# Kernel optimization log

Measured on AMD Instinct MI355X. Metric: run time of the kernel, lower is better.

The kernel has to match this reference:

```python
import jax, jax.numpy as jnp
import numpy as np

N = 16384
E = 524288
K = 16
IN_C, HID, OUT = 3, 64, 64


def _mlp(h, Wa, ba, Wb, bb):
    # Linear -> ReLU -> Linear -> ReLU (as in nn.Sequential)
    return jax.nn.relu(jax.nn.relu(h @ Wa + ba) @ Wb + bb)


def _edgeconv(x, src, dst, Wa, ba, Wb, bb, n):
    # PyG EdgeConv message: nn([x_i, x_j - x_i]) with i=dst (target), j=src (source)
    xi = x[dst]                       # [E, C]
    xj = x[src]                       # [E, C]
    m = _mlp(jnp.concatenate([xi, xj - xi], axis=-1), Wa, ba, Wb, bb)  # [E, H]
    out = jax.ops.segment_max(m, dst, num_segments=n)
    # nodes with no incoming edges: fill 0 (PyG scatter-max fill value)
    return jnp.where(jnp.isfinite(out), out, 0.0)


def _knn_edges(x, k):
    # pairwise squared distances in feature space; includes self (torch_cluster.knn(x, x, k))
    sq = jnp.sum(x * x, axis=1)                      # [N]
    dist = sq[:, None] + sq[None, :] - 2.0 * (x @ x.T)  # [N, N]
    _, idx = jax.lax.top_k(-dist, k)                 # [N, k] nearest (incl. self)
    src = idx.reshape(-1)
    dst = jnp.repeat(jnp.arange(x.shape[0]), k)
    return src, dst


def setup_inputs() -> dict:
    key = jax.random.key(0)
    ks = jax.random.split(key, 8)
    sc = lambda fan: 1.0 / np.sqrt(fan)
    return {
        "x": jax.random.normal(ks[0], (N, IN_C), dtype=jnp.float32),
        "edge_index": jax.random.randint(ks[1], (2, E), 0, N, dtype=jnp.int64),
        "k": K,
        "W1": jax.random.normal(ks[2], (2 * IN_C, HID), dtype=jnp.float32) * sc(2 * IN_C),
        "b1": jnp.zeros((HID,), dtype=jnp.float32),
        "W2": jax.random.normal(ks[3], (HID, HID), dtype=jnp.float32) * sc(HID),
        "b2": jnp.zeros((HID,), dtype=jnp.float32),
        "W3": jax.random.normal(ks[4], (2 * HID, OUT), dtype=jnp.float32) * sc(2 * HID),
        "b3": jnp.zeros((OUT,), dtype=jnp.float32),
        "W4": jax.random.normal(ks[5], (OUT, OUT), dtype=jnp.float32) * sc(OUT),
        "b4": jnp.zeros((OUT,), dtype=jnp.float32),
    }


def reference(x, edge_index, k, W1, b1, W2, b2, W3, b3, W4, b4):
    n = x.shape[0]
    # static EdgeConv (edge_index[0]=source j, edge_index[1]=target i)
    x1 = _edgeconv(x, edge_index[0], edge_index[1], W1, b1, W2, b2, n)
    # DynamicEdgeConv: kNN in feature space of x1, then EdgeConv
    src2, dst2 = _knn_edges(x1, k)
    x2 = _edgeconv(x1, src2, dst2, W3, b3, W4, b4, n)
    return x2
```

## Files before the change

### kernel.cpp

```cpp
#include <hip/hip_runtime.h>
#include <stdint.h>

#define NN   16384
#define NE   524288
#define TK   17
#define TAU  4e-5f

#define S1   2048
#define JC1  16
#define CH1  (S1 / JC1)
#define JCB  8
#define CAP  512
#define LCAP 64
#define OFB  256
#define MGNB2 1e-3f

typedef unsigned long long u64;
typedef unsigned int u32;
typedef unsigned short u16;
typedef __attribute__((ext_vector_type(8))) short bf16x8;
typedef __attribute__((ext_vector_type(4))) float f32x4;

__device__ __forceinline__ float mulrn(float a, float b) { return __fmul_rn(a, b); }
__device__ __forceinline__ float addrn(float a, float b) { return __fadd_rn(a, b); }
__device__ __forceinline__ float subrn(float a, float b) { return __fsub_rn(a, b); }

__device__ __forceinline__ u32 fkey(float f) {
    u32 b = __float_as_uint(f);
    return ((int)b < 0) ? ~b : (b | 0x80000000u);
}
__device__ __forceinline__ float inv_fkey(u32 k) {
    return (k & 0x80000000u) ? __uint_as_float(k & 0x7fffffffu) : __uint_as_float(~k);
}

__device__ __forceinline__ u16 f2bf(float f) {
    u32 x = __float_as_uint(f);
    u32 r = x + 0x7fffu + ((x >> 16) & 1u);
    return (u16)(r >> 16);
}

template<int K>
__device__ __forceinline__ void topk_insert(u64 (&key)[K], u64 nk) {
#pragma unroll
    for (int s = K - 1; s >= 1; --s) {
        bool c1 = nk < key[s - 1];
        bool c0 = nk < key[s];
        key[s] = c1 ? key[s - 1] : (c0 ? nk : key[s]);
    }
    if (nk < key[0]) key[0] = nk;
}

#define XR_DECL float4 xq0, xq1, xq2, xq3, xq4, xq5, xq6, xq7, \
                       xq8, xq9, xq10, xq11, xq12, xq13, xq14, xq15

#define XR_LOAD(ptr) do { const float4* xp_ = (const float4*)(ptr); \
    xq0  = xp_[0];  xq1  = xp_[1];  xq2  = xp_[2];  xq3  = xp_[3]; \
    xq4  = xp_[4];  xq5  = xp_[5];  xq6  = xp_[6];  xq7  = xp_[7]; \
    xq8  = xp_[8];  xq9  = xp_[9];  xq10 = xp_[10]; xq11 = xp_[11]; \
    xq12 = xp_[12]; xq13 = xp_[13]; xq14 = xp_[14]; xq15 = xp_[15]; } while (0)

#define DOT_STEP(res, qq, w_) \
    res = fmaf(qq.x, w_.x, res); res = fmaf(qq.y, w_.y, res); \
    res = fmaf(qq.z, w_.z, res); res = fmaf(qq.w, w_.w, res);

#define DOT64(res, ptr) do { const float4* jp_ = (const float4*)(ptr); \
    float4 w_ = jp_[0]; \
    res = mulrn(xq0.x, w_.x); res = fmaf(xq0.y, w_.y, res); \
    res = fmaf(xq0.z, w_.z, res); res = fmaf(xq0.w, w_.w, res); \
    w_ = jp_[1];  DOT_STEP(res, xq1,  w_) \
    w_ = jp_[2];  DOT_STEP(res, xq2,  w_) \
    w_ = jp_[3];  DOT_STEP(res, xq3,  w_) \
    w_ = jp_[4];  DOT_STEP(res, xq4,  w_) \
    w_ = jp_[5];  DOT_STEP(res, xq5,  w_) \
    w_ = jp_[6];  DOT_STEP(res, xq6,  w_) \
    w_ = jp_[7];  DOT_STEP(res, xq7,  w_) \
    w_ = jp_[8];  DOT_STEP(res, xq8,  w_) \
    w_ = jp_[9];  DOT_STEP(res, xq9,  w_) \
    w_ = jp_[10]; DOT_STEP(res, xq10, w_) \
    w_ = jp_[11]; DOT_STEP(res, xq11, w_) \
    w_ = jp_[12]; DOT_STEP(res, xq12, w_) \
    w_ = jp_[13]; DOT_STEP(res, xq13, w_) \
    w_ = jp_[14]; DOT_STEP(res, xq14, w_) \
    w_ = jp_[15]; DOT_STEP(res, xq15, w_) } while (0)

__global__ __launch_bounds__(256) void hist_kernel(const int* __restrict__ ei,
                                                   int* __restrict__ hist) {
    int e = blockIdx.x * 256 + threadIdx.x;
    atomicAdd(&hist[ei[NE + e]], 1);
}

__global__ __launch_bounds__(256) void scan_kernel(const int* __restrict__ hist,
                                                   int* __restrict__ base) {
    __shared__ int part[256];
    __shared__ int off[256];
    int t = threadIdx.x;
    int s = 0;
    for (int b = 0; b < 64; b++) s += hist[t * 64 + b];
    part[t] = s;
    __syncthreads();
    if (t == 0) {
        int run = 0;
        for (int i = 0; i < 256; i++) { off[i] = run; run += part[i]; }
    }
    __syncthreads();
    int run = off[t];
    for (int b = 0; b < 64; b++) {
        base[t * 64 + b] = run;
        run += hist[t * 64 + b];
    }
}

__global__ __launch_bounds__(256) void scatter_kernel(const int* __restrict__ ei,
                                                      int* __restrict__ base,
                                                      int* __restrict__ esrc,
                                                      int* __restrict__ edst) {
    int e = blockIdx.x * 256 + threadIdx.x;
    int d = ei[NE + e];
    int pos = atomicAdd(&base[d], 1);
    esrc[pos] = ei[e];
    edst[pos] = d;
}

__global__ __launch_bounds__(256) void conv1_np_kernel(const float* __restrict__ x,
                                                       const float* __restrict__ W1,
                                                       const float* __restrict__ b1,
                                                       const float* __restrict__ W2,
                                                       const float* __restrict__ b2,
                                                       const int* __restrict__ esrc,
                                                       const int* __restrict__ edst,
                                                       float* __restrict__ x1n) {
    __shared__ float HT[64 * 132];
    __shared__ float W1s[384];
    __shared__ float W2s[64 * 64];
    __shared__ float b1s[64], b2s[64];
    __shared__ int dsts[128];
    int t = threadIdx.x;
    int eb = blockIdx.x * 128;

    {
        const float4* w4 = (const float4*)W2;
        float4* wd = (float4*)W2s;
#pragma unroll
        for (int q = 0; q < 4; q++) wd[t + q * 256] = w4[t + q * 256];
        if (t < 96) ((float4*)W1s)[t] = ((const float4*)W1)[t];
        if (t < 64) { b1s[t] = b1[t]; b2s[t] = b2[t]; }
    }
    __syncthreads();

    {
        int el = t >> 1;
        int cb = (t & 1) * 32;
        int e = eb + el;
        int j = esrc[e];
        int i = edst[e];
        if ((t & 1) == 0) dsts[el] = i;
        float xi0 = x[i * 3 + 0], xi1 = x[i * 3 + 1], xi2 = x[i * 3 + 2];
        float xj0 = x[j * 3 + 0], xj1 = x[j * 3 + 1], xj2 = x[j * 3 + 2];
        float d0 = subrn(xj0, xi0), d1 = subrn(xj1, xi1), d2 = subrn(xj2, xi2);
#pragma unroll
        for (int cc = 0; cc < 32; cc++) {
            int c = cb + cc;
            float acc = mulrn(xi0, W1s[c]);
            acc = fmaf(xi1, W1s[64 + c], acc);
            acc = fmaf(xi2, W1s[128 + c], acc);
            acc = fmaf(d0,  W1s[192 + c], acc);
            acc = fmaf(d1,  W1s[256 + c], acc);
            acc = fmaf(d2,  W1s[320 + c], acc);
            HT[c * 132 + el] = fmaxf(addrn(acc, b1s[c]), 0.f);
        }
    }
    __syncthreads();

    int cg = t & 7, eg = t >> 3;
    int c0 = cg * 8, e0 = eg * 4;
    float acc[4][8] = {};
    for (int k = 0; k < 64; k++) {
        float4 a  = *(const float4*)&HT[k * 132 + e0];
        float4 w0 = *(const float4*)&W2s[k * 64 + c0];
        float4 w1 = *(const float4*)&W2s[k * 64 + c0 + 4];
        float av[4] = {a.x, a.y, a.z, a.w};
        float wv[8] = {w0.x, w0.y, w0.z, w0.w, w1.x, w1.y, w1.z, w1.w};
#pragma unroll
        for (int r = 0; r < 4; r++)
#pragma unroll
            for (int c = 0; c < 8; c++) acc[r][c] = fmaf(av[r], wv[c], acc[r][c]);
    }
    __syncthreads();
#pragma unroll
    for (int r = 0; r < 4; r++)
#pragma unroll
        for (int c = 0; c < 8; c++)
            HT[(c0 + c) * 132 + (e0 + r)] = fmaxf(addrn(acc[r][c], b2s[c0 + c]), 0.f);
    __syncthreads();

    {
        int col = t & 63;
        int ebeg = (t >> 6) * 32;
        const float* hp = &HT[col * 132];
        int cur = dsts[ebeg];
        float m = hp[ebeg];
        for (int e = ebeg + 1; e < ebeg + 32; e++) {
            int d2 = dsts[e];
            float v = hp[e];
            if (d2 == cur) {
                m = fmaxf(m, v);
            } else {
                atomicMax((u32*)(x1n + (size_t)cur * 64 + col), __float_as_uint(m));
                cur = d2;
                m = v;
            }
        }
        atomicMax((u32*)(x1n + (size_t)cur * 64 + col), __float_as_uint(m));
    }
}

__global__ __launch_bounds__(256) void sq_np_kernel(const float* __restrict__ x1,
                                                    float* __restrict__ sq) {
    int i = blockIdx.x * 256 + threadIdx.x;
    const float* p = x1 + (size_t)i * 64;
    float r[8];
#pragma unroll
    for (int j = 0; j < 8; j++) { float v = p[j]; r[j] = mulrn(v, v); }
#pragma unroll
    for (int b = 8; b < 64; b += 8)
#pragma unroll
        for (int j = 0; j < 8; j++) { float v = p[b + j]; r[j] = addrn(r[j], mulrn(v, v)); }
    sq[i] = addrn(addrn(addrn(r[0], r[1]), addrn(r[2], r[3])),
                  addrn(addrn(r[4], r[5]), addrn(r[6], r[7])));
}

__global__ __launch_bounds__(256) void cvt_bf_kernel(const float* __restrict__ x1,
                                                     u16* __restrict__ xb,
                                                     u16* __restrict__ xl) {
    int i = (blockIdx.x * 256 + threadIdx.x) * 8;
    uint4 oh, ol;
    u32 hw[8], lw[8];
#pragma unroll
    for (int q = 0; q < 8; q++) {
        float v = x1[i + q];
        u16 h = f2bf(v);
        float hf = __uint_as_float((u32)h << 16);
        u16 l = f2bf(subrn(v, hf));
        hw[q] = h; lw[q] = l;
    }
    oh.x = hw[0] | (hw[1] << 16); oh.y = hw[2] | (hw[3] << 16);
    oh.z = hw[4] | (hw[5] << 16); oh.w = hw[6] | (hw[7] << 16);
    ol.x = lw[0] | (lw[1] << 16); ol.y = lw[2] | (lw[3] << 16);
    ol.z = lw[4] | (lw[5] << 16); ol.w = lw[6] | (lw[7] << 16);
    *(uint4*)(xb + i) = oh;
    *(uint4*)(xl + i) = ol;
}

__global__ __launch_bounds__(256, 4) void knn_tau_kernel(const float* __restrict__ x1,
                                                         const float* __restrict__ sq,
                                                         u32* __restrict__ part1) {
    int rb = blockIdx.x >> 4;
    int ch = blockIdx.x & 15;
    int t = threadIdx.x;
    int r = rb * 256 + t;
    XR_DECL;
    XR_LOAD(x1 + (size_t)r * 64);
    float sqr = sq[r];
    u32 key[TK];
#pragma unroll
    for (int s = 0; s < TK; s++) key[s] = 0xFFFFFFFFu;
    int j0 = ch * CH1;
    for (int jj = 0; jj < CH1; jj++) {
        int j = j0 + jj;
        float a;
        DOT64(a, x1 + (size_t)j * 64);
        float dd = subrn(addrn(sqr, sq[j]), mulrn(2.f, a));
        u32 nk = fkey(dd);
#pragma unroll
        for (int s = TK - 1; s >= 1; --s) key[s] = min(max(nk, key[s - 1]), key[s]);
        key[0] = min(key[0], nk);
    }
    u32* pp = part1 + ((size_t)r * JC1 + ch) * TK;
#pragma unroll
    for (int s = 0; s < TK; s++) pp[s] = key[s];
}

__global__ __launch_bounds__(256) void tau_merge_kernel(const u32* __restrict__ part1,
                                                        float* __restrict__ tauf) {
    int r = blockIdx.x * 256 + threadIdx.x;
    u32 key[TK];
#pragma unroll
    for (int s = 0; s < TK; s++) key[s] = 0xFFFFFFFFu;
    const u32* cp = part1 + (size_t)r * (JC1 * TK);
    for (int c = 0; c < JC1; c++) {
        for (int s = 0; s < TK; s++) {
            u32 nk = cp[c * TK + s];
            if (nk >= key[TK - 1]) break;
#pragma unroll
            for (int q = TK - 1; q >= 1; --q) key[q] = min(max(nk, key[q - 1]), key[q]);
            key[0] = min(key[0], nk);
        }
    }
    tauf[r] = inv_fkey(key[TK - 1]);
}

__global__ __launch_bounds__(256, 3) void knn_collect_mfma(const u16* __restrict__ xb,
                                                           const u16* __restrict__ xl,
                                                           const float* __restrict__ sq,
                                                           const float* __restrict__ tauf,
                                                           int* __restrict__ ccnt,
                                                           u16* __restrict__ cidx) {
    __shared__ u16 slist[64 * LCAP];
    __shared__ int scnt[64];
    __shared__ int sbase[64];
    int rb = blockIdx.x >> 3;
    int jc = blockIdx.x & 7;
    int t = threadIdx.x;
    int w = t >> 6, l = t & 63;
    int lr = l & 15, lg = l >> 4;
    int rbase = rb * 64;
    if (t < 64) scnt[t] = 0;

    bf16x8 fah[4][2], fal[4][2];
#pragma unroll
    for (int rs = 0; rs < 4; rs++) {
        size_t off = (size_t)(rbase + rs * 16 + lr) * 64 + lg * 8;
        fah[rs][0] = *(const bf16x8*)(xb + off);
        fah[rs][1] = *(const bf16x8*)(xb + off + 32);
        fal[rs][0] = *(const bf16x8*)(xl + off);
        fal[rs][1] = *(const bf16x8*)(xl + off + 32);
    }
    const float BCO = 0.5f * (1.f - MGNB2);
    float thrA[16];
#pragma unroll
    for (int rs = 0; rs < 4; rs++)
#pragma unroll
        for (int i = 0; i < 4; i++) {
            int rr = rbase + rs * 16 + lg * 4 + i;
            thrA[rs * 4 + i] = 0.5f * ((1.f - MGNB2) * sq[rr] - tauf[rr]);
        }
    __syncthreads();

    const int RNG = NN / JCB / 4;
    int j0 = jc * (NN / JCB) + w * RNG;
    size_t poff = (size_t)(j0 + lr) * 64 + lg * 8;
    bf16x8 nh0 = *(const bf16x8*)(xb + poff);
    bf16x8 nh1 = *(const bf16x8*)(xb + poff + 32);
    bf16x8 nl0 = *(const bf16x8*)(xl + poff);
    bf16x8 nl1 = *(const bf16x8*)(xl + poff + 32);
    for (int js = 0; js < RNG; js += 16) {
        bf16x8 fbh0 = nh0, fbh1 = nh1, fbl0 = nl0, fbl1 = nl1;
        int jb = j0 + js;
        int jsn = (js + 16 < RNG) ? js + 16 : js;
        size_t noff = (size_t)(j0 + jsn + lr) * 64 + lg * 8;
        nh0 = *(const bf16x8*)(xb + noff);
        nh1 = *(const bf16x8*)(xb + noff + 32);
        nl0 = *(const bf16x8*)(xl + noff);
        nl1 = *(const bf16x8*)(xl + noff + 32);
        int j = jb + lr;
        float thB = BCO * sq[j];
#pragma unroll
        for (int rs = 0; rs < 4; rs++) {
            f32x4 acc = {0.f, 0.f, 0.f, 0.f};
            acc = __builtin_amdgcn_mfma_f32_16x16x32_bf16(fah[rs][0], fbh0, acc, 0, 0, 0);
            acc = __builtin_amdgcn_mfma_f32_16x16x32_bf16(fah[rs][1], fbh1, acc, 0, 0, 0);
            acc = __builtin_amdgcn_mfma_f32_16x16x32_bf16(fah[rs][0], fbl0, acc, 0, 0, 0);
            acc = __builtin_amdgcn_mfma_f32_16x16x32_bf16(fah[rs][1], fbl1, acc, 0, 0, 0);
            acc = __builtin_amdgcn_mfma_f32_16x16x32_bf16(fal[rs][0], fbh0, acc, 0, 0, 0);
            acc = __builtin_amdgcn_mfma_f32_16x16x32_bf16(fal[rs][1], fbh1, acc, 0, 0, 0);
#pragma unroll
            for (int i = 0; i < 4; i++) {
                if (acc[i] >= thrA[rs * 4 + i] + thB) {
                    int rl = rs * 16 + lg * 4 + i;
                    int slot = atomicAdd(&scnt[rl], 1);
                    if (slot < LCAP) {
                        slist[rl * LCAP + slot] = (u16)j;
                    } else {
                        int rr = rbase + rl;
                        int gslot = atomicAdd(&ccnt[rr], 1);
                        if (gslot < CAP) cidx[(size_t)rr * CAP + gslot] = (u16)j;
                    }
                }
            }
        }
    }
    __syncthreads();

    if (t < 64) {
        int ldsn = min(scnt[t], LCAP);
        sbase[t] = (ldsn > 0) ? atomicAdd(&ccnt[rbase + t], ldsn) : -1;
    }
    __syncthreads();
    {
        int rl = t >> 2, ln = t & 3;
        int ldsn = min(scnt[rl], LCAP);
        int base = sbase[rl];
        if (base >= 0) {
            for (int s = ln; s < ldsn; s += 4) {
                int dst = base + s;
                if (dst < CAP)
                    cidx[(size_t)(rbase + rl) * CAP + dst] = slist[rl * LCAP + s];
            }
        }
    }
}

__global__ __launch_bounds__(256) void oflow_scan_kernel(const int* __restrict__ ccnt,
                                                         int* __restrict__ ocnt,
                                                         int* __restrict__ olist) {
    int r = blockIdx.x * 256 + threadIdx.x;
    if (ccnt[r] > CAP) {
        int s = atomicAdd(ocnt, 1);
        olist[s] = r;
    }
}

__global__ __launch_bounds__(256, 2) void oflow_fix_kernel(const float* __restrict__ x1,
                                                           const float* __restrict__ sq,
                                                           const int* __restrict__ ocnt,
                                                           const int* __restrict__ olist,
                                                           u16* __restrict__ cidx,
                                                           int* __restrict__ ccnt) {
    __shared__ u64 m[256 * TK];
    int nof = *ocnt;
    int t = threadIdx.x;
    for (int w = blockIdx.x; w < nof; w += gridDim.x) {
        int r = olist[w];
        XR_DECL;
        XR_LOAD(x1 + (size_t)r * 64);
        float sqr = sq[r];
        u64 key[TK];
#pragma unroll
        for (int s = 0; s < TK; s++) key[s] = ~0ull;
        for (int j = t; j < NN; j += 256) {
            float a;
            DOT64(a, x1 + (size_t)j * 64);
            float dd = subrn(addrn(sqr, sq[j]), mulrn(2.f, a));
            u64 nk = ((u64)fkey(dd) << 32) | (u32)j;
            if (nk < key[TK - 1]) topk_insert<TK>(key, nk);
        }
#pragma unroll
        for (int s = 0; s < TK; s++) m[t * TK + s] = key[s];
        __syncthreads();
        if (t == 0) {
            u64 fin[TK];
#pragma unroll
            for (int s = 0; s < TK; s++) fin[s] = ~0ull;
            for (int l = 0; l < 256; l++)
                for (int s = 0; s < TK; s++) {
                    u64 nk = m[l * TK + s];
                    if (nk >= fin[TK - 1]) break;
                    topk_insert<TK>(fin, nk);
                }
            for (int s = 0; s < TK; s++) cidx[(size_t)r * CAP + s] = (u16)(fin[s] & 0xffffu);
            ccnt[r] = TK;
        }
        __syncthreads();
    }
}

__global__ __launch_bounds__(256) void sel_row_kernel(const float* __restrict__ x1,
                                                      const float* __restrict__ sq,
                                                      const u16* __restrict__ cidx,
                                                      const int* __restrict__ ccnt,
                                                      int* __restrict__ nidxA,
                                                      int* __restrict__ nidxB,
                                                      int* __restrict__ flist,
                                                      int* __restrict__ cnt) {
    __shared__ __align__(16) u64 KL[CAP];
    __shared__ float SD[2];
    int r = blockIdx.x;
    int t = threadIdx.x;
    int cn = min(ccnt[r], CAP);
    XR_DECL;
    XR_LOAD(x1 + (size_t)r * 64);
    float sqr = sq[r];

    int s0 = t, s1 = t + 256;
    u64 k0 = ~0ull, k1 = ~0ull;
    if (s0 < cn) {
        int j = cidx[(size_t)r * CAP + s0];
        float a;
        DOT64(a, x1 + (size_t)j * 64);
        float dd = subrn(addrn(sqr, sq[j]), mulrn(2.f, a));
        k0 = ((u64)fkey(dd) << 32) | (u32)j;
        KL[s0] = k0;
    }
    if (s1 < cn) {
        int j = cidx[(size_t)r * CAP + s1];
        float a;
        DOT64(a, x1 + (size_t)j * 64);
        float dd = subrn(addrn(sqr, sq[j]), mulrn(2.f, a));
        k1 = ((u64)fkey(dd) << 32) | (u32)j;
        KL[s1] = k1;
    }
    __syncthreads();

    int r0 = 0, r1 = 0;
    bool waveLive = ((t & ~63) < cn);
    if (waveLive) {
        const ulonglong2* KL2 = (const ulonglong2*)KL;
        if (cn <= 256) {
            int q = 0;
            for (; q + 4 <= cn; q += 4) {
                ulonglong2 ab = KL2[q >> 1];
                ulonglong2 cd = KL2[(q >> 1) + 1];
                r0 += (int)(ab.x < k0) + (int)(ab.y < k0)
                    + (int)(cd.x < k0) + (int)(cd.y < k0);
            }
            for (; q < cn; q++) r0 += (KL[q] < k0);
        } else {
            int q = 0;
            for (; q + 4 <= cn; q += 4) {
                ulonglong2 ab = KL2[q >> 1];
                ulonglong2 cd = KL2[(q >> 1) + 1];
                r0 += (int)(ab.x < k0) + (int)(ab.y < k0)
                    + (int)(cd.x < k0) + (int)(cd.y < k0);
                r1 += (int)(ab.x < k1) + (int)(ab.y < k1)
                    + (int)(cd.x < k1) + (int)(cd.y < k1);
            }
            for (; q < cn; q++) { u64 kq = KL[q]; r0 += (kq < k0); r1 += (kq < k1); }
        }
    }

    if (s0 < cn && r0 < TK) {
        int j = (int)(k0 & 0xffffffffu);
        if (r0 < 16) nidxA[r * 16 + r0] = j;
        if (r0 < 15) nidxB[r * 16 + r0] = j;
        if (r0 == 16) nidxB[r * 16 + 15] = j;
        if (r0 == 15) SD[0] = inv_fkey((u32)(k0 >> 32));
        if (r0 == 16) SD[1] = inv_fkey((u32)(k0 >> 32));
    }
    if (s1 < cn && r1 < TK) {
        int j = (int)(k1 & 0xffffffffu);
        if (r1 < 16) nidxA[r * 16 + r1] = j;
        if (r1 < 15) nidxB[r * 16 + r1] = j;
        if (r1 == 16) nidxB[r * 16 + 15] = j;
        if (r1 == 15) SD[0] = inv_fkey((u32)(k1 >> 32));
        if (r1 == 16) SD[1] = inv_fkey((u32)(k1 >> 32));
    }
    __syncthreads();
    if (t == 0) {
        if (SD[1] - SD[0] <= TAU) {
            int s = atomicAdd(cnt, 1);
            flist[s] = r;
        }
    }
}

__global__ __launch_bounds__(256) void pq2_kernel(const float* __restrict__ x1,
                                                  const float* __restrict__ W3,
                                                  float* __restrict__ P,
                                                  float* __restrict__ Q) {
    __shared__ float XT[64 * 68];
    __shared__ float W3s[128 * 64];
    int t = threadIdx.x;
    int rb = blockIdx.x * 64;
    {
        const float4* w4 = (const float4*)W3;
        float4* wd = (float4*)W3s;
#pragma unroll
        for (int q = 0; q < 8; q++) wd[t + q * 256] = w4[t + q * 256];
    }
    {
        int rl = t >> 2, cb = (t & 3) * 16;
        const float4* xs = (const float4*)(x1 + (size_t)(rb + rl) * 64 + cb);
#pragma unroll
        for (int q4 = 0; q4 < 4; q4++) {
            float4 v = xs[q4];
            int c = cb + q4 * 4;
            XT[(c + 0) * 68 + rl] = v.x;
            XT[(c + 1) * 68 + rl] = v.y;
            XT[(c + 2) * 68 + rl] = v.z;
            XT[(c + 3) * 68 + rl] = v.w;
        }
    }
    __syncthreads();

    int cg = t & 15, rg = t >> 4;
    int c0 = cg * 8, r0 = rg * 4;
    float acc[4][8] = {};
    for (int k = 0; k < 64; k++) {
        float4 a = *(const float4*)&XT[k * 68 + r0];
        int wb = (c0 < 64) ? (k * 64 + c0) : ((64 + k) * 64 + (c0 - 64));
        float4 w0 = *(const float4*)&W3s[wb];
        float4 w1 = *(const float4*)&W3s[wb + 4];
        float av[4] = {a.x, a.y, a.z, a.w};
        float wv[8] = {w0.x, w0.y, w0.z, w0.w, w1.x, w1.y, w1.z, w1.w};
#pragma unroll
        for (int r = 0; r < 4; r++)
#pragma unroll
            for (int c = 0; c < 8; c++) acc[r][c] = fmaf(av[r], wv[c], acc[r][c]);
    }
    float* base = (c0 < 64) ? P : Q;
    int cc = c0 & 63;
#pragma unroll
    for (int r = 0; r < 4; r++) {
        float* op = base + (size_t)(rb + r0 + r) * 64 + cc;
        *(float4*)(op)     = make_float4(acc[r][0], acc[r][1], acc[r][2], acc[r][3]);
        *(float4*)(op + 4) = make_float4(acc[r][4], acc[r][5], acc[r][6], acc[r][7]);
    }
}

__global__ __launch_bounds__(256) void conv2_kernel(const float* __restrict__ P,
                                                    const float* __restrict__ Q,
                                                    const float* __restrict__ b3,
                                                    const float* __restrict__ W4,
                                                    const float* __restrict__ b4,
                                                    const int* __restrict__ idx,
                                                    float* __restrict__ out) {
    __shared__ float HT[64 * 132];
    __shared__ float W4s[64 * 64];
    __shared__ float b4s[64];
    int t = threadIdx.x;
    int nb = blockIdx.x * 8;
    int eb = nb * 16;
    {
        const float4* w4 = (const float4*)W4;
        float4* wd = (float4*)W4s;
#pragma unroll
        for (int q = 0; q < 4; q++) wd[t + q * 256] = w4[t + q * 256];
        if (t < 64) b4s[t] = b4[t];
    }
    {
        int el = t >> 1;
        int qh = (t & 1) * 32;
        int i = nb + (el >> 4);
        int j = idx[eb + el];
        const float4* Pi = (const float4*)(P + (size_t)i * 64 + qh);
        const float4* Qi = (const float4*)(Q + (size_t)i * 64 + qh);
        const float4* Qj = (const float4*)(Q + (size_t)j * 64 + qh);
        const float4* bv = (const float4*)(b3 + qh);
#pragma unroll
        for (int q4 = 0; q4 < 8; q4++) {
            float4 p = Pi[q4], qi = Qi[q4], qj = Qj[q4], bb = bv[q4];
            int q = qh + q4 * 4;
            HT[(q + 0) * 132 + el] = fmaxf(bb.x + p.x + qj.x - qi.x, 0.f);
            HT[(q + 1) * 132 + el] = fmaxf(bb.y + p.y + qj.y - qi.y, 0.f);
            HT[(q + 2) * 132 + el] = fmaxf(bb.z + p.z + qj.z - qi.z, 0.f);
            HT[(q + 3) * 132 + el] = fmaxf(bb.w + p.w + qj.w - qi.w, 0.f);
        }
    }
    __syncthreads();

    int nl = t >> 5;
    int c0 = (t & 31) * 2;
    float acc[16][2];
#pragma unroll
    for (int r = 0; r < 16; r++) { acc[r][0] = 0.f; acc[r][1] = 0.f; }
    for (int k = 0; k < 64; k++) {
        const float* hp = &HT[k * 132 + nl * 16];
        float4 a0 = *(const float4*)(hp);
        float4 a1 = *(const float4*)(hp + 4);
        float4 a2 = *(const float4*)(hp + 8);
        float4 a3 = *(const float4*)(hp + 12);
        float2 w = *(const float2*)&W4s[k * 64 + c0];
        float av[16] = {a0.x, a0.y, a0.z, a0.w, a1.x, a1.y, a1.z, a1.w,
                        a2.x, a2.y, a2.z, a2.w, a3.x, a3.y, a3.z, a3.w};
#pragma unroll
        for (int r = 0; r < 16; r++) {
            acc[r][0] = fmaf(av[r], w.x, acc[r][0]);
            acc[r][1] = fmaf(av[r], w.y, acc[r][1]);
        }
    }
    float m0 = acc[0][0], m1 = acc[0][1];
#pragma unroll
    for (int r = 1; r < 16; r++) { m0 = fmaxf(m0, acc[r][0]); m1 = fmaxf(m1, acc[r][1]); }
    m0 = fmaxf(m0 + b4s[c0], 0.f);
    m1 = fmaxf(m1 + b4s[c0 + 1], 0.f);
    *(float2*)&out[(size_t)(nb + nl) * 64 + c0] = make_float2(m0, m1);
}

__global__ __launch_bounds__(256) void conv2b_kernel(const float* __restrict__ P,
                                                     const float* __restrict__ Q,
                                                     const float* __restrict__ b3,
                                                     const float* __restrict__ W4,
                                                     const float* __restrict__ b4,
                                                     const int* __restrict__ idxB,
                                                     const int* __restrict__ flist,
                                                     const int* __restrict__ cnt,
                                                     float* __restrict__ out) {
    int nfl = *cnt;
    int base = blockIdx.x * 8;
    if (base >= nfl) return;

    __shared__ float HT[64 * 132];
    __shared__ float W4s[64 * 64];
    __shared__ float b4s[64];
    int t = threadIdx.x;
    {
        const float4* w4 = (const float4*)W4;
        float4* wd = (float4*)W4s;
#pragma unroll
        for (int q = 0; q < 4; q++) wd[t + q * 256] = w4[t + q * 256];
        if (t < 64) b4s[t] = b4[t];
    }
    {
        int el = t >> 1;
        int qh = (t & 1) * 32;
        int slot = base + (el >> 4);
        int i = (slot < nfl) ? flist[slot] : flist[base];
        int j = idxB[i * 16 + (el & 15)];
        const float4* Pi = (const float4*)(P + (size_t)i * 64 + qh);
        const float4* Qi = (const float4*)(Q + (size_t)i * 64 + qh);
        const float4* Qj = (const float4*)(Q + (size_t)j * 64 + qh);
        const float4* bv = (const float4*)(b3 + qh);
#pragma unroll
        for (int q4 = 0; q4 < 8; q4++) {
            float4 p = Pi[q4], qi = Qi[q4], qj = Qj[q4], bb = bv[q4];
            int q = qh + q4 * 4;
            HT[(q + 0) * 132 + el] = fmaxf(bb.x + p.x + qj.x - qi.x, 0.f);
            HT[(q + 1) * 132 + el] = fmaxf(bb.y + p.y + qj.y - qi.y, 0.f);
            HT[(q + 2) * 132 + el] = fmaxf(bb.z + p.z + qj.z - qi.z, 0.f);
            HT[(q + 3) * 132 + el] = fmaxf(bb.w + p.w + qj.w - qi.w, 0.f);
        }
    }
    __syncthreads();

    int nl = t >> 5;
    int c0 = (t & 31) * 2;
    float acc[16][2];
#pragma unroll
    for (int r = 0; r < 16; r++) { acc[r][0] = 0.f; acc[r][1] = 0.f; }
    for (int k = 0; k < 64; k++) {
        const float* hp = &HT[k * 132 + nl * 16];
        float4 a0 = *(const float4*)(hp);
        float4 a1 = *(const float4*)(hp + 4);
        float4 a2 = *(const float4*)(hp + 8);
        float4 a3 = *(const float4*)(hp + 12);
        float2 w = *(const float2*)&W4s[k * 64 + c0];
        float av[16] = {a0.x, a0.y, a0.z, a0.w, a1.x, a1.y, a1.z, a1.w,
                        a2.x, a2.y, a2.z, a2.w, a3.x, a3.y, a3.z, a3.w};
#pragma unroll
        for (int r = 0; r < 16; r++) {
            acc[r][0] = fmaf(av[r], w.x, acc[r][0]);
            acc[r][1] = fmaf(av[r], w.y, acc[r][1]);
        }
    }
    float m0 = acc[0][0], m1 = acc[0][1];
#pragma unroll
    for (int r = 1; r < 16; r++) { m0 = fmaxf(m0, acc[r][0]); m1 = fmaxf(m1, acc[r][1]); }
    m0 = fmaxf(m0 + b4s[c0], 0.f);
    m1 = fmaxf(m1 + b4s[c0 + 1], 0.f);

    int slot2 = base + nl;
    if (slot2 < nfl) {
        int i2 = flist[slot2];
        float* op = out + (size_t)i2 * 64 + c0;
        float2 old = *(float2*)op;
        *(float2*)op = make_float2(0.5f * (old.x + m0), 0.5f * (old.y + m1));
    }
}

extern "C" void kernel_launch(void* const* d_in, const int* in_sizes, int n_in,
                              void* d_out, int out_size, void* d_ws, size_t ws_size,
                              hipStream_t stream) {
    const float* x  = (const float*)d_in[0];
    const int*   ei = (const int*)d_in[1];
    const float* W1 = (const float*)d_in[3];
    const float* b1 = (const float*)d_in[4];
    const float* W2 = (const float*)d_in[5];
    const float* b2 = (const float*)d_in[6];
    const float* W3 = (const float*)d_in[7];
    const float* b3 = (const float*)d_in[8];
    const float* W4 = (const float*)d_in[9];
    const float* b4 = (const float*)d_in[10];
    float* out = (float*)d_out;

    char* ws = (char*)d_ws;
    float* x1f   = (float*)(ws);
    float* sqf   = (float*)(ws + 4194304);
    float* tauf  = (float*)(ws + 4259840);
    int*   ccnt  = (int*)(ws + 4325376);
    int*   ocnt  = (int*)(ws + 6422528);
    int*   fcnt  = (int*)(ws + 6422592);
    int*   olist = (int*)(ws + 6422656);
    int*   flist = (int*)(ws + 6488192);
    int*   nidxA = (int*)(ws + 6553728);
    int*   nidxB = (int*)(ws + 7602304);
    u32*   part1 = (u32*)(ws + 8650880);
    u16*   cidx  = (u16*)(ws + 8650880);
    float* Pf    = (float*)(ws + 8650880);
    float* Qf    = (float*)(ws + 12845184);
    int*   esrc  = (int*)(ws + 26476672);
    u16*   x1bf  = (u16*)(ws + 26476672);
    int*   edst  = (int*)(ws + 28573824);
    u16*   x1bflo = (u16*)(ws + 28573824);
    int*   hist  = (int*)(ws + 30670976);

    hipMemsetAsync(x1f, 0, (size_t)NN * 64 * sizeof(float), stream);
    hipMemsetAsync(ccnt, 0, NN * sizeof(int), stream);
    hipMemsetAsync(ocnt, 0, 128, stream);
    hipMemsetAsync(hist, 0, NN * sizeof(int), stream);

    hist_kernel<<<NE / 256, 256, 0, stream>>>(ei, hist);
    scan_kernel<<<1, 256, 0, stream>>>(hist, hist);
    scatter_kernel<<<NE / 256, 256, 0, stream>>>(ei, hist, esrc, edst);

    conv1_np_kernel<<<NE / 128, 256, 0, stream>>>(x, W1, b1, W2, b2, esrc, edst, x1f);
    sq_np_kernel<<<NN / 256, 256, 0, stream>>>(x1f, sqf);

    knn_tau_kernel<<<(NN / 256) * JC1, 256, 0, stream>>>(x1f, sqf, part1);
    tau_merge_kernel<<<NN / 256, 256, 0, stream>>>(part1, tauf);

    cvt_bf_kernel<<<NN * 64 / 8 / 256, 256, 0, stream>>>(x1f, x1bf, x1bflo);
    knn_collect_mfma<<<(NN / 64) * JCB, 256, 0, stream>>>(x1bf, x1bflo, sqf, tauf, ccnt, cidx);
    oflow_scan_kernel<<<NN / 256, 256, 0, stream>>>(ccnt, ocnt, olist);
    oflow_fix_kernel<<<OFB, 256, 0, stream>>>(x1f, sqf, ocnt, olist, cidx, ccnt);
    sel_row_kernel<<<NN, 256, 0, stream>>>(x1f, sqf, cidx, ccnt, nidxA, nidxB, flist, fcnt);

    pq2_kernel<<<NN / 64, 256, 0, stream>>>(x1f, W3, Pf, Qf);
    conv2_kernel<<<NN / 8, 256, 0, stream>>>(Pf, Qf, b3, W4, b4, nidxA, out);
    conv2b_kernel<<<NN / 8, 256, 0, stream>>>(Pf, Qf, b3, W4, b4, nidxB, flist, fcnt, out);
}
```

Before: 654.2 us.

## Compute kNN threshold with split-bf16 MFMA and in-block merge

Replaces the scalar fp32 per-thread dot-product tau kernel and its separate merge kernel with one MFMA kernel. It computes distances against the first 2048 candidates using hi/lo bf16 split products, keeps a top-17 per lane and merges the lanes in shared memory. The threshold gets a relative margin so it stays conservative under bf16 error. This removes a kernel launch and the partial-list round trip through global memory, but the threshold may be looser and admit more candidates into the collect stage.

New measurement: 651.8 us (median of 2 runs). Within noise of the previous version (-0.4%).

```diff
diff --git a/kernel.cpp b/kernel.cpp
--- a/kernel.cpp
+++ b/kernel.cpp
@@ -7,8 +7,6 @@
 #define TAU  4e-5f
 
 #define S1   2048
-#define JC1  16
-#define CH1  (S1 / JC1)
 #define JCB  8
 #define CAP  512
 #define LCAP 64
@@ -251,52 +249,83 @@
     *(uint4*)(xl + i) = ol;
 }
 
-__global__ __launch_bounds__(256, 4) void knn_tau_kernel(const float* __restrict__ x1,
-                                                         const float* __restrict__ sq,
-                                                         u32* __restrict__ part1) {
-    int rb = blockIdx.x >> 4;
-    int ch = blockIdx.x & 15;
+__global__ __launch_bounds__(256, 3) void knn_tau_mfma(const u16* __restrict__ xb,
+                                                       const u16* __restrict__ xl,
+                                                       const float* __restrict__ sq,
+                                                       float* __restrict__ tauf) {
+    __shared__ u32 KL[256 * TK];
     int t = threadIdx.x;
-    int r = rb * 256 + t;
-    XR_DECL;
-    XR_LOAD(x1 + (size_t)r * 64);
-    float sqr = sq[r];
+    int w = t >> 6, l = t & 63;
+    int lr = l & 15, lg = l >> 4;
+    int rbase = blockIdx.x * 64;
+    int myrow = rbase + w * 16 + lr;
+
+    size_t roff = (size_t)myrow * 64 + lg * 8;
+    bf16x8 fbh0 = *(const bf16x8*)(xb + roff);
+    bf16x8 fbh1 = *(const bf16x8*)(xb + roff + 32);
+    bf16x8 fbl0 = *(const bf16x8*)(xl + roff);
+    bf16x8 fbl1 = *(const bf16x8*)(xl + roff + 32);
+    float sqr = sq[myrow];
+
     u32 key[TK];
 #pragma unroll
     for (int s = 0; s < TK; s++) key[s] = 0xFFFFFFFFu;
-    int j0 = ch * CH1;
-    for (int jj = 0; jj < CH1; jj++) {
-        int j = j0 + jj;
-        float a;
-        DOT64(a, x1 + (size_t)j * 64);
-        float dd = subrn(addrn(sqr, sq[j]), mulrn(2.f, a));
-        u32 nk = fkey(dd);
-#pragma unroll
-        for (int s = TK - 1; s >= 1; --s) key[s] = min(max(nk, key[s - 1]), key[s]);
-        key[0] = min(key[0], nk);
-    }
-    u32* pp = part1 + ((size_t)r * JC1 + ch) * TK;
-#pragma unroll
-    for (int s = 0; s < TK; s++) pp[s] = key[s];
-}
-
-__global__ __launch_bounds__(256) void tau_merge_kernel(const u32* __restrict__ part1,
-                                                        float* __restrict__ tauf) {
-    int r = blockIdx.x * 256 + threadIdx.x;
-    u32 key[TK];
-#pragma unroll
-    for (int s = 0; s < TK; s++) key[s] = 0xFFFFFFFFu;
-    const u32* cp = part1 + (size_t)r * (JC1 * TK);
-    for (int c = 0; c < JC1; c++) {
-        for (int s = 0; s < TK; s++) {
-            u32 nk = cp[c * TK + s];
-            if (nk >= key[TK - 1]) break;
-#pragma unroll
-            for (int q = TK - 1; q >= 1; --q) key[q] = min(max(nk, key[q - 1]), key[q]);
-            key[0] = min(key[0], nk);
-        }
-    }
-    tauf[r] = inv_fkey(key[TK - 1]);
+
+    size_t poff = (size_t)lr * 64 + lg * 8;
+    bf16x8 nh0 = *(const bf16x8*)(xb + poff);
+    bf16x8 nh1 = *(const bf16x8*)(xb + poff + 32);
+    bf16x8 nl0 = *(const bf16x8*)(xl + poff);
+    bf16x8 nl1 = *(const bf16x8*)(xl + poff + 32);
+    for (int jt = 0; jt < S1; jt += 16) {
+        bf16x8 fah0 = nh0, fah1 = nh1, fal0 = nl0, fal1 = nl1;
+        int jtn = (jt + 16 < S1) ? jt + 16 : jt;
+        size_t noff = (size_t)(jtn + lr) * 64 + lg * 8;
+        nh0 = *(const bf16x8*)(xb + noff);
+        nh1 = *(const bf16x8*)(xb + noff + 32);
+        nl0 = *(const bf16x8*)(xl + noff);
+        nl1 = *(const bf16x8*)(xl + noff + 32);
+        f32x4 acc = {0.f, 0.f, 0.f, 0.f};
+        acc = __builtin_amdgcn_mfma_f32_16x16x32_bf16(fah0, fbh0, acc, 0, 0, 0);
+        acc = __builtin_amdgcn_mfma_f32_16x16x32_bf16(fah1, fbh1, acc, 0, 0, 0);
+        acc = __builtin_amdgcn_mfma_f32_16x16x32_bf16(fah0, fbl0, acc, 0, 0, 0);
+        acc = __builtin_amdgcn_mfma_f32_16x16x32_bf16(fah1, fbl1, acc, 0, 0, 0);
+        acc = __builtin_amdgcn_mfma_f32_16x16x32_bf16(fal0, fbh0, acc, 0, 0, 0);
+        acc = __builtin_amdgcn_mfma_f32_16x16x32_bf16(fal1, fbh1, acc, 0, 0, 0);
+        float4 sq4 = *(const float4*)(sq + jt + lg * 4);
+        float sqj[4] = {sq4.x, sq4.y, sq4.z, sq4.w};
+#pragma unroll
+        for (int i = 0; i < 4; i++) {
+            float ss = sqr + sqj[i];
+            float dd = ss - 2.f * acc[i];
+            float v = dd + MGNB2 * ss;
+            u32 nk = fkey(v);
+            if (nk < key[TK - 1]) {
+#pragma unroll
+                for (int s = TK - 1; s >= 1; --s) key[s] = min(max(nk, key[s - 1]), key[s]);
+                key[0] = min(key[0], nk);
+            }
+        }
+    }
+#pragma unroll
+    for (int s = 0; s < TK; s++) KL[t * TK + s] = key[s];
+    __syncthreads();
+    if (t < 64) {
+        int wv = t >> 4, lrr = t & 15;
+        u32 fin[TK];
+#pragma unroll
+        for (int s = 0; s < TK; s++) fin[s] = 0xFFFFFFFFu;
+        for (int g = 0; g < 4; g++) {
+            const u32* cp = &KL[(wv * 64 + g * 16 + lrr) * TK];
+            for (int s = 0; s < TK; s++) {
+                u32 nk = cp[s];
+                if (nk >= fin[TK - 1]) break;
+#pragma unroll
+                for (int q = TK - 1; q >= 1; --q) fin[q] = min(max(nk, fin[q - 1]), fin[q]);
+                fin[0] = min(fin[0], nk);
+            }
+        }
+        tauf[rbase + wv * 16 + lrr] = inv_fkey(fin[TK - 1]);
+    }
 }
 
 __global__ __launch_bounds__(256, 3) void knn_collect_mfma(const u16* __restrict__ xb,
@@ -773,7 +802,6 @@
     int*   flist = (int*)(ws + 6488192);
     int*   nidxA = (int*)(ws + 6553728);
     int*   nidxB = (int*)(ws + 7602304);
-    u32*   part1 = (u32*)(ws + 8650880);
     u16*   cidx  = (u16*)(ws + 8650880);
     float* Pf    = (float*)(ws + 8650880);
     float* Qf    = (float*)(ws + 12845184);
@@ -795,10 +823,8 @@
     conv1_np_kernel<<<NE / 128, 256, 0, stream>>>(x, W1, b1, W2, b2, esrc, edst, x1f);
     sq_np_kernel<<<NN / 256, 256, 0, stream>>>(x1f, sqf);
 
-    knn_tau_kernel<<<(NN / 256) * JC1, 256, 0, stream>>>(x1f, sqf, part1);
-    tau_merge_kernel<<<NN / 256, 256, 0, stream>>>(part1, tauf);
-
     cvt_bf_kernel<<<NN * 64 / 8 / 256, 256, 0, stream>>>(x1f, x1bf, x1bflo);
+    knn_tau_mfma<<<NN / 64, 256, 0, stream>>>(x1bf, x1bflo, sqf, tauf);
     knn_collect_mfma<<<(NN / 64) * JCB, 256, 0, stream>>>(x1bf, x1bflo, sqf, tauf, ccnt, cidx);
     oflow_scan_kernel<<<NN / 256, 256, 0, stream>>>(ccnt, ocnt, olist);
     oflow_fix_kernel<<<OFB, 256, 0, stream>>>(x1f, sqf, ocnt, olist, cidx, ccnt);
```
